# Performance work log

Measured on AMD Instinct MI355X. Metric: run time of the kernel, lower is better.

The kernel has to match this reference:

```python
import jax, jax.numpy as jnp
import numpy as np

B, N, D = 2, 8192, 32
RADIUS2 = 0.03 ** 2
SIM_THRESH = 0.7
MIN_LEAF = 10
EPS = 1e-8


def setup_inputs() -> dict:
    key = jax.random.key(0)
    ks = jax.random.split(key, 5)
    # points scaled to [0, 0.4)^3 so the 0.03 radius finds a few neighbors per point
    points = jax.random.uniform(ks[0], (B, N, 3), dtype=jnp.float32) * 0.4
    embeddings = jax.random.normal(ks[1], (B, N, D), dtype=jnp.float32)
    leaf_mask = jax.random.randint(ks[2], (B, N), 0, 2).astype(jnp.int32)
    # consistency_net: Linear(2D -> D), ReLU, Linear(D -> D); stored as (in, out)
    W1 = jax.random.normal(ks[3], (2 * D, D), dtype=jnp.float32) / np.sqrt(2 * D)
    b1 = jnp.zeros((D,), dtype=jnp.float32)
    W2 = jax.random.normal(ks[4], (D, D), dtype=jnp.float32) / np.sqrt(D)
    b2 = jnp.zeros((D,), dtype=jnp.float32)
    return {"points": points, "embeddings": embeddings, "leaf_mask": leaf_mask,
            "W1": W1, "b1": b1, "W2": W2, "b2": b2}


def reference(points, embeddings, leaf_mask, W1, b1, W2, b2):
    leaf = leaf_mask > 0  # [B,N]
    # squared pairwise distances via ||a||^2 + ||b||^2 - 2 a.b (avoids [B,N,N,3])
    sq = jnp.sum(points * points, axis=-1)  # [B,N]
    d2 = sq[:, :, None] + sq[:, None, :] - 2.0 * jnp.einsum('bnc,bmc->bnm', points, points)
    nb = (d2 < RADIUS2) & leaf[:, None, :]  # neighbor j must be a leaf point
    nb_count = jnp.sum(nb, axis=-1)  # includes self when leaf[i]
    # cosine similarity with per-vector norm clamp (torch F.cosine_similarity eps)
    norms = jnp.maximum(jnp.linalg.norm(embeddings, axis=-1, keepdims=True), EPS)
    en = embeddings / norms
    sim = jnp.einsum('bnd,bmd->bnm', en, en)
    similar = nb & (sim > SIM_THRESH)
    cnt = jnp.sum(similar, axis=-1)  # [B,N]
    w = similar.astype(embeddings.dtype)
    mean_sim = jnp.einsum('bnm,bmd->bnd', w, embeddings) / jnp.maximum(cnt, 1)[..., None]
    combined = jnp.concatenate([embeddings, mean_sim], axis=-1)  # [B,N,2D]
    h = jax.nn.relu(combined @ W1 + b1)
    out = h @ W2 + b2
    batch_ok = (jnp.sum(leaf, axis=-1) >= MIN_LEAF)[:, None]  # skip batches with <10 leaves
    cond = leaf & (nb_count > 1) & (cnt > 0) & batch_ok
    return jnp.where(cond[..., None], out, embeddings)
```

## Files before the change

kernel.cpp:

```cpp
#include <hip/hip_runtime.h>

#define NPTS 8192
#define BN   16384
#define D    32
#define R2   0.0009f
#define SIMT 0.7f
#define RAD  0.03f
#define BLOCK 256
#define PBLOCK 1024
#define PWAVES 16
#define NGRP   (BN / 64)
#define ZBINS 512
#define ZSCALE 1280.0f
#define AFIELDS 34
#define CHUNK 512

#define GLOBAL_AS __attribute__((address_space(1)))
#define LDS_AS    __attribute__((address_space(3)))

__device__ __forceinline__ void g2lds16(const void* g, void* l) {
  __builtin_amdgcn_global_load_lds((const GLOBAL_AS void*)g, (LDS_AS void*)l,
                                   16, 0, 0);
}

__global__ __launch_bounds__(BLOCK) void histscan_kernel(
    const float* __restrict__ pts, const float* __restrict__ emb,
    const int* __restrict__ leaf, float* __restrict__ invn,
    int* __restrict__ histA, int* __restrict__ histL,
    int* __restrict__ leafcnt, unsigned* __restrict__ done,
    int* __restrict__ rsA, int* __restrict__ rsL,
    int* __restrict__ curA, int* __restrict__ curL) {
  const int p = blockIdx.x * BLOCK + threadIdx.x;
  const float z = pts[3 * p + 2];
  int bin = (int)(z * ZSCALE); if (bin > ZBINS - 1) bin = ZBINS - 1;
  const int b = p >> 13;
  const int lf = leaf[p] > 0;
  atomicAdd(&histA[b * ZBINS + bin], 1);
  if (lf) atomicAdd(&histL[b * ZBINS + bin], 1);

  const float4* er = (const float4*)(emb + (size_t)p * D);
  float ss = 0.f;
#pragma unroll
  for (int i = 0; i < D / 4; ++i) {
    float4 v = er[i];
    ss += v.x * v.x + v.y * v.y + v.z * v.z + v.w * v.w;
  }
  invn[p] = 1.0f / fmaxf(sqrtf(ss), 1e-8f);

  const unsigned long long m = __ballot(lf);
  if ((threadIdx.x & 63) == 0) atomicAdd(&leafcnt[b], (int)__popcll(m));

  __shared__ int islast;
  __threadfence();
  if (threadIdx.x == 0) {
    const unsigned t = __hip_atomic_fetch_add(done, 1u, __ATOMIC_ACQ_REL,
                                              __HIP_MEMORY_SCOPE_AGENT);
    islast = (t == gridDim.x - 1);
  }
  __syncthreads();
  if (!islast) return;

  const int wv = threadIdx.x >> 6;
  const int lane = threadIdx.x & 63;
  const int sb = wv & 1;
  const int* __restrict__ h = (wv < 2) ? histA : histL;
  int* __restrict__ rs = (wv < 2) ? rsA : rsL;
  int* __restrict__ cu = (wv < 2) ? curA : curL;
  int carry = 0;
  for (int c = 0; c < ZBINS / 64; ++c) {
    const int idx = c * 64 + lane;
    const int v = __hip_atomic_load(&h[sb * ZBINS + idx], __ATOMIC_RELAXED,
                                    __HIP_MEMORY_SCOPE_AGENT);
    int incl = v;
#pragma unroll
    for (int off = 1; off < 64; off <<= 1) {
      const int t = __shfl_up(incl, off);
      if (lane >= off) incl += t;
    }
    const int excl = carry + incl - v;
    rs[sb * (ZBINS + 1) + idx] = excl;
    cu[sb * ZBINS + idx] = excl;
    carry += __shfl(incl, 63);
  }
  if (lane == 0) rs[sb * (ZBINS + 1) + ZBINS] = carry;
}

__global__ __launch_bounds__(BLOCK) void scatter_kernel(
    const float* __restrict__ pts, const float* __restrict__ emb,
    const int* __restrict__ leaf, const float* __restrict__ invn,
    int* __restrict__ curA, int* __restrict__ curL,
    float4* __restrict__ sortedA, int* __restrict__ permA,
    float4* __restrict__ pts4L, float* __restrict__ invL,
    float* __restrict__ embL) {
  const int p = blockIdx.x * BLOCK + threadIdx.x;
  const float x = pts[3 * p + 0];
  const float y = pts[3 * p + 1];
  const float z = pts[3 * p + 2];
  const float sq = x * x + y * y + z * z;
  const int lf = leaf[p] > 0;
  const float inv = invn[p];
  int bin = (int)(z * ZSCALE); if (bin > ZBINS - 1) bin = ZBINS - 1;
  const int b = p >> 13;

  const int dst = b * NPTS + atomicAdd(&curA[b * ZBINS + bin], 1);
  sortedA[dst] = make_float4(x, y, z, lf ? inv : -inv);
  permA[dst] = p;

  if (lf) {
    const int dl = b * NPTS + atomicAdd(&curL[b * ZBINS + bin], 1);
    pts4L[dl] = make_float4(x, y, z, 0.5f * (sq - R2));
    invL[dl] = inv;
    const float4* __restrict__ s4 = (const float4*)(emb + (size_t)p * D);
    float4* __restrict__ d4 = (float4*)(embL + (size_t)dl * D);
#pragma unroll
    for (int k = 0; k < D / 4; ++k) d4[k] = s4[k];
  }
}

__global__ __launch_bounds__(PBLOCK) void pair_kernel(
    const float4* __restrict__ sortedA, const int* __restrict__ permA,
    const float4* __restrict__ pts4L, const float* __restrict__ invL,
    const float* __restrict__ embL, const float* __restrict__ emb,
    const int* __restrict__ rsL, const int* __restrict__ leafcnt,
    const float* __restrict__ W1, const float* __restrict__ b1,
    const float* __restrict__ W2, const float* __restrict__ b2,
    float* __restrict__ out) {
  const int ig   = blockIdx.x;
  const int b    = ig >> 7;
  const int lane = threadIdx.x & 63;
  const int wv   = threadIdx.x >> 6;
  const int sg   = ig * 64 + lane;

  __shared__ __align__(16) float4 ptsS[2][CHUNK];
  __shared__ __align__(16) float4 eiS4[64 * 8];
  __shared__ float invIS[64];
  __shared__ int   queueS[PWAVES][128];
  __shared__ float red[AFIELDS][64];
  for (int t = threadIdx.x; t < AFIELDS * 64; t += PBLOCK)
    (&red[0][0])[t] = 0.f;

  const float4 A = sortedA[sg];
  const float inv_i = fabsf(A.w);
  const float mhsq = -0.5f * (A.x * A.x + A.y * A.y + A.z * A.z);
  const int p = permA[sg];

  if (wv == 0) {
    const float4* __restrict__ e4 = (const float4*)(emb + (size_t)p * D);
#pragma unroll
    for (int k = 0; k < D / 4; ++k) eiS4[lane * 8 + (k ^ (lane & 7))] = e4[k];
    invIS[lane] = inv_i;
  }

  float zmin = A.z, zmax = A.z;
#pragma unroll
  for (int off = 1; off < 64; off <<= 1) {
    zmin = fminf(zmin, __shfl_xor(zmin, off));
    zmax = fmaxf(zmax, __shfl_xor(zmax, off));
  }
  int klo = (int)((zmin - RAD) * ZSCALE) - 1; if (klo < 0) klo = 0;
  int khi = (int)((zmax + RAD) * ZSCALE) + 1; if (khi > ZBINS - 1) khi = ZBINS - 1;
  klo = __builtin_amdgcn_readfirstlane(klo);
  khi = __builtin_amdgcn_readfirstlane(khi);
  const int jlo = b * NPTS + rsL[b * (ZBINS + 1) + klo];
  const int jhi = b * NPTS + rsL[b * (ZBINS + 1) + khi + 1];
  const int len = jhi - jlo;

  float nbc = 0.f;
  int qtail = 0, qdone = 0;

  const float4* __restrict__ embQ = (const float4*)embL;

  auto drain = [&](int n) {
    if (lane < n) {
      const int e  = queueS[wv][(qdone + lane) & 127];
      const int il = e & 63;
      const int j  = e >> 6;
      float4 bv[D / 4];
#pragma unroll
      for (int k = 0; k < D / 4; ++k) bv[k] = embQ[(size_t)j * 8 + k];
      const float invj = invL[j];
      float s0 = 0.f, s1 = 0.f, s2 = 0.f, s3 = 0.f;
#pragma unroll
      for (int k = 0; k < D / 4; ++k) {
        const float4 av = eiS4[il * 8 + (k ^ (il & 7))];
        s0 = fmaf(av.x, bv[k].x, s0);
        s1 = fmaf(av.y, bv[k].y, s1);
        s2 = fmaf(av.z, bv[k].z, s2);
        s3 = fmaf(av.w, bv[k].w, s3);
      }
      const float sim = ((s0 + s1) + (s2 + s3)) * invIS[il] * invj;
      if (sim > SIMT) {
        atomicAdd(&red[1][il], 1.0f);
#pragma unroll
        for (int k = 0; k < D / 4; ++k) {
          atomicAdd(&red[2 + 4 * k + 0][il], bv[k].x);
          atomicAdd(&red[2 + 4 * k + 1][il], bv[k].y);
          atomicAdd(&red[2 + 4 * k + 2][il], bv[k].z);
          atomicAdd(&red[2 + 4 * k + 3][il], bv[k].w);
        }
      }
    }
    qdone += n;
  };

  auto stage = [&](int buf, int base, int L) {
    for (int t0 = wv * 64; t0 < L; t0 += PWAVES * 64)
      g2lds16((const char*)pts4L + (((size_t)(base + t0 + lane)) << 4),
              &ptsS[buf][t0]);
  };

  auto process = [&](int buf, int jbase, int L) {
    const int s0 = (L * wv) / PWAVES;
    const int s1 = (L * (wv + 1)) / PWAVES;
    if (s0 >= s1) return;
    float4 c = ptsS[buf][s0];
    for (int jl = s0; jl < s1; ++jl) {
      const float4 cn = ptsS[buf][(jl + 1 < s1) ? (jl + 1) : s0];
      const float t = fmaf(A.z, c.z, fmaf(A.y, c.y, fmaf(A.x, c.x, mhsq)));
      const bool hit = t > c.w;
      const unsigned long long m = __ballot(hit);
      if (m) {
        if (hit) {
          nbc += 1.0f;
          const int below = __popcll(m & ((1ull << lane) - 1ull));
          queueS[wv][(qtail + below) & 127] = ((jbase + jl) << 6) | lane;
        }
        qtail += (int)__popcll(m);
        if (qtail - qdone >= 64) drain(64);
      }
      c = cn;
    }
  };

  const int nch = (len + CHUNK - 1) / CHUNK;
  if (nch > 0) stage(0, jlo, (len < CHUNK) ? len : CHUNK);
  __syncthreads();
  for (int k = 0; k < nch; ++k) {
    const int cur = k & 1;
    if (k + 1 < nch) {
      const int base = jlo + (k + 1) * CHUNK;
      const int L = (jhi - base < CHUNK) ? (jhi - base) : CHUNK;
      stage(cur ^ 1, base, L);
    }
    const int base = jlo + k * CHUNK;
    const int Lc = (jhi - base < CHUNK) ? (jhi - base) : CHUNK;
    process(cur, base, Lc);
    __syncthreads();
  }
  drain(qtail - qdone);

  if (nbc != 0.f) atomicAdd(&red[0][lane], nbc);
  __syncthreads();

  if (threadIdx.x < 64) {
    const float tnbc = red[0][lane];
    const float tcnt = red[1][lane];
    const float rinv = 1.0f / fmaxf(tcnt, 1.0f);

    float e[D];
#pragma unroll
    for (int k = 0; k < D / 4; ++k) {
      const float4 v = eiS4[lane * 8 + (k ^ (lane & 7))];
      e[4 * k + 0] = v.x; e[4 * k + 1] = v.y;
      e[4 * k + 2] = v.z; e[4 * k + 3] = v.w;
    }

    float h[D];
#pragma unroll
    for (int k = 0; k < D; ++k) h[k] = b1[k];
    for (int d = 0; d < D; ++d) {
      const float c = e[d];
      const float* __restrict__ w = W1 + (size_t)d * D;
#pragma unroll
      for (int k = 0; k < D; ++k) h[k] = fmaf(c, w[k], h[k]);
    }
    for (int d = 0; d < D; ++d) {
      const float c = red[2 + d][lane] * rinv;
      const float* __restrict__ w = W1 + (size_t)(D + d) * D;
#pragma unroll
      for (int k = 0; k < D; ++k) h[k] = fmaf(c, w[k], h[k]);
    }
#pragma unroll
    for (int k = 0; k < D; ++k) h[k] = fmaxf(h[k], 0.f);

    float o[D];
#pragma unroll
    for (int m = 0; m < D; ++m) o[m] = b2[m];
    for (int k = 0; k < D; ++k) {
      const float c = h[k];
      const float* __restrict__ w = W2 + (size_t)k * D;
#pragma unroll
      for (int m = 0; m < D; ++m) o[m] = fmaf(c, w[m], o[m]);
    }

    const bool lf = A.w > 0.f;
    const bool cond = lf && (tnbc >= 2.0f) && (tcnt >= 1.0f) && (leafcnt[b] >= 10);

    float4* outr = (float4*)(out + (size_t)p * D);
#pragma unroll
    for (int i = 0; i < D / 4; ++i) {
      float4 v;
      if (cond) { v.x = o[4*i+0]; v.y = o[4*i+1]; v.z = o[4*i+2]; v.w = o[4*i+3]; }
      else      { v.x = e[4*i+0]; v.y = e[4*i+1]; v.z = e[4*i+2]; v.w = e[4*i+3]; }
      outr[i] = v;
    }
  }
}

extern "C" void kernel_launch(void* const* d_in, const int* in_sizes, int n_in,
                              void* d_out, int out_size, void* d_ws, size_t ws_size,
                              hipStream_t stream) {
  (void)in_sizes; (void)n_in; (void)out_size; (void)ws_size;
  const float* pts  = (const float*)d_in[0];
  const float* emb  = (const float*)d_in[1];
  const int*   leaf = (const int*)d_in[2];
  const float* W1   = (const float*)d_in[3];
  const float* b1   = (const float*)d_in[4];
  const float* W2   = (const float*)d_in[5];
  const float* b2   = (const float*)d_in[6];
  float* out = (float*)d_out;

  char* ws = (char*)d_ws;
  size_t off = 0;
  auto alloc = [&](size_t bytes) { void* r = ws + off; off = (off + bytes + 15) & ~(size_t)15; return r; };

  float4*   sortedA = (float4*)alloc((size_t)BN * 16);
  int*      permA   = (int*)alloc((size_t)BN * 4);
  float4*   pts4L   = (float4*)alloc((size_t)(BN + CHUNK) * 16);
  float*    invL    = (float*)alloc((size_t)(BN + CHUNK) * 4);
  float*    embL    = (float*)alloc((size_t)(BN + CHUNK) * D * 4);
  float*    invn    = (float*)alloc((size_t)BN * 4);
  int*      rsA     = (int*)alloc(2 * (ZBINS + 1) * 4);
  int*      rsL     = (int*)alloc(2 * (ZBINS + 1) * 4);
  int*      curA    = (int*)alloc(2 * ZBINS * 4);
  int*      curL    = (int*)alloc(2 * ZBINS * 4);
  int*      histA   = (int*)alloc(2 * ZBINS * 4);
  int*      histL   = (int*)alloc(2 * ZBINS * 4);
  int*      leafcnt = (int*)alloc(16);
  unsigned* done    = (unsigned*)alloc(16);

  hipMemsetAsync(histA, 0, 2 * (2 * ZBINS * 4) + 32, stream);
  histscan_kernel<<<BN / BLOCK, BLOCK, 0, stream>>>(
      pts, emb, leaf, invn, histA, histL, leafcnt, done, rsA, rsL, curA, curL);
  scatter_kernel<<<BN / BLOCK, BLOCK, 0, stream>>>(
      pts, emb, leaf, invn, curA, curL, sortedA, permA, pts4L, invL, embL);
  pair_kernel<<<NGRP, PBLOCK, 0, stream>>>(
      sortedA, permA, pts4L, invL, embL, emb, rsL, leafcnt,
      W1, b1, W2, b2, out);
}
```

Measured before the change: 115.1 us.

## Fuse histogram/scan and scatter kernels with a grid-wide spin barrier

The histogram+scan kernel and the scatter kernel are merged into one prep kernel. The last block to finish performs the prefix scan and publishes a flag, and all other blocks spin-wait on it before scattering. Embeddings stay in registers, so the invn buffer and the second embedding read go away, and the leaf count is taken from the scan total instead of a separate atomic counter. This removes one kernel launch and a round trip through global memory. The cost is a grid-wide barrier that depends on all 64 blocks being co-resident, which holds on this GPU.

Result: slower. 117.6 us (+2.2%).

```diff
diff --git a/kernel.cpp b/kernel.cpp
--- a/kernel.cpp
+++ b/kernel.cpp
@@ -23,71 +23,12 @@
                                    16, 0, 0);
 }
 
-__global__ __launch_bounds__(BLOCK) void histscan_kernel(
+__global__ __launch_bounds__(BLOCK) void prep_kernel(
     const float* __restrict__ pts, const float* __restrict__ emb,
-    const int* __restrict__ leaf, float* __restrict__ invn,
+    const int* __restrict__ leaf,
     int* __restrict__ histA, int* __restrict__ histL,
-    int* __restrict__ leafcnt, unsigned* __restrict__ done,
+    unsigned* __restrict__ done,
     int* __restrict__ rsA, int* __restrict__ rsL,
-    int* __restrict__ curA, int* __restrict__ curL) {
-  const int p = blockIdx.x * BLOCK + threadIdx.x;
-  const float z = pts[3 * p + 2];
-  int bin = (int)(z * ZSCALE); if (bin > ZBINS - 1) bin = ZBINS - 1;
-  const int b = p >> 13;
-  const int lf = leaf[p] > 0;
-  atomicAdd(&histA[b * ZBINS + bin], 1);
-  if (lf) atomicAdd(&histL[b * ZBINS + bin], 1);
-
-  const float4* er = (const float4*)(emb + (size_t)p * D);
-  float ss = 0.f;
-#pragma unroll
-  for (int i = 0; i < D / 4; ++i) {
-    float4 v = er[i];
-    ss += v.x * v.x + v.y * v.y + v.z * v.z + v.w * v.w;
-  }
-  invn[p] = 1.0f / fmaxf(sqrtf(ss), 1e-8f);
-
-  const unsigned long long m = __ballot(lf);
-  if ((threadIdx.x & 63) == 0) atomicAdd(&leafcnt[b], (int)__popcll(m));
-
-  __shared__ int islast;
-  __threadfence();
-  if (threadIdx.x == 0) {
-    const unsigned t = __hip_atomic_fetch_add(done, 1u, __ATOMIC_ACQ_REL,
-                                              __HIP_MEMORY_SCOPE_AGENT);
-    islast = (t == gridDim.x - 1);
-  }
-  __syncthreads();
-  if (!islast) return;
-
-  const int wv = threadIdx.x >> 6;
-  const int lane = threadIdx.x & 63;
-  const int sb = wv & 1;
-  const int* __restrict__ h = (wv < 2) ? histA : histL;
-  int* __restrict__ rs = (wv < 2) ? rsA : rsL;
-  int* __restrict__ cu = (wv < 2) ? curA : curL;
-  int carry = 0;
-  for (int c = 0; c < ZBINS / 64; ++c) {
-    const int idx = c * 64 + lane;
-    const int v = __hip_atomic_load(&h[sb * ZBINS + idx], __ATOMIC_RELAXED,
-                                    __HIP_MEMORY_SCOPE_AGENT);
-    int incl = v;
-#pragma unroll
-    for (int off = 1; off < 64; off <<= 1) {
-      const int t = __shfl_up(incl, off);
-      if (lane >= off) incl += t;
-    }
-    const int excl = carry + incl - v;
-    rs[sb * (ZBINS + 1) + idx] = excl;
-    cu[sb * ZBINS + idx] = excl;
-    carry += __shfl(incl, 63);
-  }
-  if (lane == 0) rs[sb * (ZBINS + 1) + ZBINS] = carry;
-}
-
-__global__ __launch_bounds__(BLOCK) void scatter_kernel(
-    const float* __restrict__ pts, const float* __restrict__ emb,
-    const int* __restrict__ leaf, const float* __restrict__ invn,
     int* __restrict__ curA, int* __restrict__ curL,
     float4* __restrict__ sortedA, int* __restrict__ permA,
     float4* __restrict__ pts4L, float* __restrict__ invL,
@@ -97,10 +38,71 @@
   const float y = pts[3 * p + 1];
   const float z = pts[3 * p + 2];
   const float sq = x * x + y * y + z * z;
-  const int lf = leaf[p] > 0;
-  const float inv = invn[p];
   int bin = (int)(z * ZSCALE); if (bin > ZBINS - 1) bin = ZBINS - 1;
   const int b = p >> 13;
+  const int lf = leaf[p] > 0;
+  atomicAdd(&histA[b * ZBINS + bin], 1);
+  if (lf) atomicAdd(&histL[b * ZBINS + bin], 1);
+
+  float4 er[D / 4];
+  float ss = 0.f;
+  {
+    const float4* __restrict__ e4 = (const float4*)(emb + (size_t)p * D);
+#pragma unroll
+    for (int i = 0; i < D / 4; ++i) {
+      er[i] = e4[i];
+      ss += er[i].x * er[i].x + er[i].y * er[i].y +
+            er[i].z * er[i].z + er[i].w * er[i].w;
+    }
+  }
+  const float inv = 1.0f / fmaxf(sqrtf(ss), 1e-8f);
+
+  __shared__ int islast;
+  __threadfence();
+  if (threadIdx.x == 0) {
+    const unsigned t = __hip_atomic_fetch_add(&done[0], 1u, __ATOMIC_ACQ_REL,
+                                              __HIP_MEMORY_SCOPE_AGENT);
+    islast = (t == gridDim.x - 1);
+  }
+  __syncthreads();
+
+  if (islast) {
+    const int wv = threadIdx.x >> 6;
+    const int lane = threadIdx.x & 63;
+    const int sb = wv & 1;
+    const int* __restrict__ h = (wv < 2) ? histA : histL;
+    int* __restrict__ rs = (wv < 2) ? rsA : rsL;
+    int* __restrict__ cu = (wv < 2) ? curA : curL;
+    int carry = 0;
+    for (int c = 0; c < ZBINS / 64; ++c) {
+      const int idx = c * 64 + lane;
+      const int v = __hip_atomic_load(&h[sb * ZBINS + idx], __ATOMIC_RELAXED,
+                                      __HIP_MEMORY_SCOPE_AGENT);
+      int incl = v;
+#pragma unroll
+      for (int off = 1; off < 64; off <<= 1) {
+        const int t = __shfl_up(incl, off);
+        if (lane >= off) incl += t;
+      }
+      const int excl = carry + incl - v;
+      rs[sb * (ZBINS + 1) + idx] = excl;
+      cu[sb * ZBINS + idx] = excl;
+      carry += __shfl(incl, 63);
+    }
+    if (lane == 0) rs[sb * (ZBINS + 1) + ZBINS] = carry;
+    __threadfence();
+    __syncthreads();
+    if (threadIdx.x == 0)
+      __hip_atomic_store(&done[1], 1u, __ATOMIC_RELEASE,
+                         __HIP_MEMORY_SCOPE_AGENT);
+  } else {
+    if (threadIdx.x == 0) {
+      while (__hip_atomic_load(&done[1], __ATOMIC_ACQUIRE,
+                               __HIP_MEMORY_SCOPE_AGENT) == 0)
+        __builtin_amdgcn_s_sleep(8);
+    }
+    __syncthreads();
+  }
 
   const int dst = b * NPTS + atomicAdd(&curA[b * ZBINS + bin], 1);
   sortedA[dst] = make_float4(x, y, z, lf ? inv : -inv);
@@ -110,10 +112,9 @@
     const int dl = b * NPTS + atomicAdd(&curL[b * ZBINS + bin], 1);
     pts4L[dl] = make_float4(x, y, z, 0.5f * (sq - R2));
     invL[dl] = inv;
-    const float4* __restrict__ s4 = (const float4*)(emb + (size_t)p * D);
     float4* __restrict__ d4 = (float4*)(embL + (size_t)dl * D);
 #pragma unroll
-    for (int k = 0; k < D / 4; ++k) d4[k] = s4[k];
+    for (int k = 0; k < D / 4; ++k) d4[k] = er[k];
   }
 }
 
@@ -121,7 +122,7 @@
     const float4* __restrict__ sortedA, const int* __restrict__ permA,
     const float4* __restrict__ pts4L, const float* __restrict__ invL,
     const float* __restrict__ embL, const float* __restrict__ emb,
-    const int* __restrict__ rsL, const int* __restrict__ leafcnt,
+    const int* __restrict__ rsL,
     const float* __restrict__ W1, const float* __restrict__ b1,
     const float* __restrict__ W2, const float* __restrict__ b2,
     float* __restrict__ out) {
@@ -294,7 +295,8 @@
     }
 
     const bool lf = A.w > 0.f;
-    const bool cond = lf && (tnbc >= 2.0f) && (tcnt >= 1.0f) && (leafcnt[b] >= 10);
+    const int nleaf = rsL[b * (ZBINS + 1) + ZBINS];
+    const bool cond = lf && (tnbc >= 2.0f) && (tcnt >= 1.0f) && (nleaf >= 10);
 
     float4* outr = (float4*)(out + (size_t)p * D);
 #pragma unroll
@@ -329,22 +331,19 @@
   float4*   pts4L   = (float4*)alloc((size_t)(BN + CHUNK) * 16);
   float*    invL    = (float*)alloc((size_t)(BN + CHUNK) * 4);
   float*    embL    = (float*)alloc((size_t)(BN + CHUNK) * D * 4);
-  float*    invn    = (float*)alloc((size_t)BN * 4);
   int*      rsA     = (int*)alloc(2 * (ZBINS + 1) * 4);
   int*      rsL     = (int*)alloc(2 * (ZBINS + 1) * 4);
   int*      curA    = (int*)alloc(2 * ZBINS * 4);
   int*      curL    = (int*)alloc(2 * ZBINS * 4);
   int*      histA   = (int*)alloc(2 * ZBINS * 4);
   int*      histL   = (int*)alloc(2 * ZBINS * 4);
-  int*      leafcnt = (int*)alloc(16);
   unsigned* done    = (unsigned*)alloc(16);
 
-  hipMemsetAsync(histA, 0, 2 * (2 * ZBINS * 4) + 32, stream);
-  histscan_kernel<<<BN / BLOCK, BLOCK, 0, stream>>>(
-      pts, emb, leaf, invn, histA, histL, leafcnt, done, rsA, rsL, curA, curL);
-  scatter_kernel<<<BN / BLOCK, BLOCK, 0, stream>>>(
-      pts, emb, leaf, invn, curA, curL, sortedA, permA, pts4L, invL, embL);
+  hipMemsetAsync(histA, 0, 2 * (2 * ZBINS * 4) + 16, stream);
+  prep_kernel<<<BN / BLOCK, BLOCK, 0, stream>>>(
+      pts, emb, leaf, histA, histL, done, rsA, rsL, curA, curL,
+      sortedA, permA, pts4L, invL, embL);
   pair_kernel<<<NGRP, PBLOCK, 0, stream>>>(
-      sortedA, permA, pts4L, invL, embL, emb, rsL, leafcnt,
+      sortedA, permA, pts4L, invL, embL, emb, rsL,
       W1, b1, W2, b2, out);
 }
```
